# Kernel optimization log

Hardware: AMD Instinct MI355X
Metric: run time of the kernel (lower is better)

The kernel has to match this reference:

```python
import jax, jax.numpy as jnp
import numpy as np

VOCAB, SEQ, D_EMB, D_HID, BATCH = 50257, 256, 256, 512, 16

def setup_inputs() -> dict:
    key = jax.random.key(0)
    ks = jax.random.split(key, 8)
    s_e = 1.0 / np.sqrt(D_EMB)
    s_h = 1.0 / np.sqrt(D_HID)
    return {
        "idx": jax.random.randint(ks[0], (BATCH, SEQ), 0, VOCAB),
        "E":  jax.random.normal(ks[1], (VOCAB, D_EMB), jnp.float32) * 0.02,
        "Wi": jax.random.normal(ks[2], (D_EMB, 4 * D_HID), jnp.float32) * s_e,  # input kernel (no bias in flax LSTMCell)
        "Wh": jax.random.normal(ks[3], (D_HID, 4 * D_HID), jnp.float32) * s_h,  # recurrent kernel
        "bh": jnp.zeros((4 * D_HID,), jnp.float32),                              # recurrent bias
        "Wo": jax.random.normal(ks[4], (D_HID, VOCAB), jnp.float32) * s_h,
        "bo": jnp.zeros((VOCAB,), jnp.float32),
    }

def reference(idx, E, Wi, Wh, bh, Wo, bo):
    B, S = idx.shape
    H = Wh.shape[0]
    x = E[idx]                                   # [B, S, D] embedding gather
    # precompute input contribution for all timesteps: [S, B, 4H]
    xz = jnp.einsum('bsd,dg->sbg', x, Wi)

    def step(carry, xz_t):
        h, c = carry
        z = xz_t + h @ Wh + bh                   # [B, 4H]
        i, f, g, o = jnp.split(z, 4, axis=-1)    # flax gate order: i, f, g, o
        i = jax.nn.sigmoid(i)
        f = jax.nn.sigmoid(f)
        g = jnp.tanh(g)
        o = jax.nn.sigmoid(o)
        c = f * c + i * g
        h = o * jnp.tanh(c)
        return (h, c), h

    h0 = jnp.zeros((B, H), x.dtype)
    c0 = jnp.zeros((B, H), x.dtype)
    _, hs = jax.lax.scan(step, (h0, c0), xz)     # hs: [S, B, H]
    hs = jnp.transpose(hs, (1, 0, 2))            # [B, S, H]
    logits = hs @ Wo + bo                        # [B, S, V]
    return logits
```

## Files before the change

kernel.cpp:

```cpp
#include <hip/hip_runtime.h>
#include <cstdint>


typedef __attribute__((ext_vector_type(8))) short short8;
typedef __attribute__((ext_vector_type(4))) float f32x4;
typedef __attribute__((ext_vector_type(4))) unsigned int u32x4;
typedef __attribute__((ext_vector_type(4))) unsigned short ush4;

#define DEVFN static __device__ __forceinline__

DEVFN unsigned short f2bf(float f) {
    unsigned int u = __float_as_uint(f);
    return (unsigned short)((u + 0x7FFFu + ((u >> 16) & 1u)) >> 16);
}
DEVFN float bf2f(unsigned short h) { return __uint_as_float(((unsigned int)h) << 16); }
DEVFN float sigm(float x) { return 1.0f / (1.0f + __expf(-x)); }
DEVFN float tanh_fast(float x) {
    float e = __expf(-2.0f * fabsf(x));
    float t = (1.0f - e) / (1.0f + e);
    return copysignf(t, x);
}
DEVFN f32x4 fzero() { f32x4 v = {0.f, 0.f, 0.f, 0.f}; return v; }

DEVFN void aload16(u32x4& d, const void* p) {
    asm volatile("global_load_dwordx4 %0, %1, off sc0 sc1" : "=v"(d) : "v"(p));
}

__global__ __launch_bounds__(256) void k0_wot(const float* __restrict__ Wo,
                                              uint32_t* __restrict__ WoTP) {
    __shared__ float tile[32][33];
    const int bx = blockIdx.x;
    const int cb = bx >> 4;
    const int kb = bx & 15;
    const int c0 = cb * 32, k0 = kb * 32;
    const int j = threadIdx.x & 31;
    const int i0 = threadIdx.x >> 5;
    for (int ii = i0; ii < 32; ii += 8) {
        const int c = c0 + j;
        tile[ii][j] = (c < 50257) ? Wo[(size_t)(k0 + ii) * 50257 + c] : 0.0f;
    }
    __syncthreads();
    for (int ii = i0; ii < 32; ii += 8) {
        const float v = tile[j][ii];
        const unsigned short hi = f2bf(v);
        const unsigned short lo = f2bf(v - bf2f(hi));
        WoTP[(size_t)(c0 + ii) * 512 + k0 + j] = (((unsigned int)hi) << 16) | lo;
    }
}

__global__ __launch_bounds__(256) void k0b_whlo(const float* __restrict__ Wh,
                                                uint32_t* __restrict__ WLO) {
    const int tid = blockIdx.x * 256 + threadIdx.x;
    const int lane = tid & 63;
    const int q    = (tid >> 6) & 15;
    const int nt   = (tid >> 10) & 1;
    const int wg   = tid >> 11;
    const int cc   = lane & 15;
    const int gcol = (cc >> 2) * 512 + wg * 8 + nt * 4 + (cc & 3);
    const int kbase = q * 32 + (lane >> 4) * 8;
    u32x4 o;
#pragma unroll
    for (int p = 0; p < 4; ++p) {
        unsigned int pair = 0;
#pragma unroll
        for (int e = 0; e < 2; ++e) {
            const int k = kbase + p * 2 + e;
            const float w = Wh[(size_t)k * 2048 + gcol];
            const unsigned short hi = f2bf(w);
            const unsigned short lo = f2bf(w - bf2f(hi));
            pair |= ((unsigned int)lo) << (e * 16);
        }
        o[p] = pair;
    }
    *(u32x4*)(WLO + (size_t)tid * 4) = o;
}

__global__ __launch_bounds__(256) void k1_xz(const int* __restrict__ idx,
                                             const float* __restrict__ E,
                                             const float* __restrict__ Wi,
                                             unsigned short* __restrict__ xzH) {
    __shared__ float xs[16][256];
    const int s = blockIdx.x;
    const int t = threadIdx.x;
#pragma unroll
    for (int b = 0; b < 16; ++b) {
        const int row = idx[b * 256 + s];
        xs[b][t] = E[(size_t)row * 256 + t];
    }
    __syncthreads();
    for (int half = 0; half < 2; ++half) {
        const int g0 = half * 1024 + t * 4;
        f32x4 acc[16];
#pragma unroll
        for (int b = 0; b < 16; ++b) acc[b] = fzero();
        for (int d = 0; d < 256; ++d) {
            const f32x4 w = *(const f32x4*)&Wi[(size_t)d * 2048 + g0];
#pragma unroll
            for (int b = 0; b < 16; ++b) {
                const float xv = xs[b][d];
                acc[b] += xv * w;
            }
        }
#pragma unroll
        for (int b = 0; b < 16; ++b) {
            ush4 o;
#pragma unroll
            for (int jj = 0; jj < 4; ++jj) o[jj] = f2bf(acc[b][jj]);
            *(ush4*)&xzH[((size_t)s * 16 + b) * 2048 + g0] = o;
        }
    }
}

__global__ __launch_bounds__(256, 1) void k23(const float* __restrict__ Wh,
                                              const float* __restrict__ bh,
                                              const unsigned short* __restrict__ xzH,
                                              const short8* __restrict__ WLO8,
                                              uint32_t* __restrict__ hsP,
                                              const uint32_t* __restrict__ zeroh,
                                              uint32_t* __restrict__ flags,
                                              const uint32_t* __restrict__ WoTP,
                                              const float* __restrict__ bo,
                                              float* __restrict__ out) {
    __shared__ __align__(16) char smem[98304];

    if (blockIdx.x < 64) {
        const int wg = blockIdx.x;
        const int tid = threadIdx.x;

        unsigned short* whh = (unsigned short*)smem;

        {
            const int l = tid >> 3, seg = tid & 7;
            const int cc = l & 15, nt0 = l >> 4;
            const int gcol = (cc >> 2) * 512 + wg * 8 + nt0 * 4 + (cc & 3);
            for (int k8 = seg * 64; k8 < seg * 64 + 64; k8 += 8) {
                short8 v;
#pragma unroll
                for (int i = 0; i < 8; ++i)
                    v[i] = (short)f2bf(Wh[(size_t)(k8 + i) * 2048 + gcol]);
                const int slot = (k8 >> 3) ^ (l & 7);
                *(short8*)((char*)whh + l * 1024 + slot * 16) = v;
            }
        }
        __syncthreads();
        if (tid >= 64) return;

        const int lane = tid;
        const int c = lane & 15;
        const int qtr = lane >> 4;

        int gc[2];
        float bh_v[2];
#pragma unroll
        for (int nt = 0; nt < 2; ++nt) {
            gc[nt] = (c >> 2) * 512 + wg * 8 + nt * 4 + (c & 3);
            bh_v[nt] = bh[gc[nt]];
        }
        float cst[2][4];
#pragma unroll
        for (int nt = 0; nt < 2; ++nt)
#pragma unroll
            for (int r = 0; r < 4; ++r) cst[nt][r] = 0.0f;

        float xzv[2][4];
#pragma unroll
        for (int nt = 0; nt < 2; ++nt)
#pragma unroll
            for (int r = 0; r < 4; ++r)
                xzv[nt][r] = bf2f(xzH[(size_t)(qtr * 4 + r) * 2048 + gc[nt]]);

        const uint32_t* flg = flags + lane;

        short8 bz = {0, 0, 0, 0, 0, 0, 0, 0};
        f32x4 bd0 = fzero(), bd1 = fzero();

        for (int t = 0; t < 256; ++t) {
            if (t > 0) {
                while (true) {
                    const uint32_t v = __hip_atomic_load(flg, __ATOMIC_RELAXED,
                                                         __HIP_MEMORY_SCOPE_AGENT);
                    if (__all((int)(v >= (uint32_t)t))) break;
#pragma unroll
                    for (int i = 0; i < 4; ++i) {
                        bd0 = __builtin_amdgcn_mfma_f32_16x16x32_bf16(bz, bz, bd0, 0, 0, 0);
                        bd1 = __builtin_amdgcn_mfma_f32_16x16x32_bf16(bz, bz, bd1, 0, 0, 0);
                    }
                }
                __builtin_amdgcn_sched_barrier(0);
            }

            const uint32_t* hbase = (t == 0)
                ? (zeroh + (size_t)c * 512)
                : (hsP + ((size_t)(t - 1) * 16 + c) * 512);

            f32x4 acc[2][2];
#pragma unroll
            for (int nt = 0; nt < 2; ++nt) { acc[nt][0] = fzero(); acc[nt][1] = fzero(); }

#pragma unroll
            for (int q = 0; q < 16; ++q) {
                const int kb = q * 32 + qtr * 8;
                const unsigned long long* hb64 = (const unsigned long long*)(hbase + kb);
                unsigned long long d[4];
#pragma unroll
                for (int i = 0; i < 4; ++i)
                    d[i] = __hip_atomic_load(hb64 + i, __ATOMIC_RELAXED,
                                             __HIP_MEMORY_SCOPE_AGENT);
                short8 ahi, alo;
#pragma unroll
                for (int i = 0; i < 4; ++i) {
                    const uint32_t wlo32 = (uint32_t)d[i];
                    const uint32_t whi32 = (uint32_t)(d[i] >> 32);
                    ahi[2 * i]     = (short)(wlo32 >> 16); alo[2 * i]     = (short)(wlo32 & 0xffffu);
                    ahi[2 * i + 1] = (short)(whi32 >> 16); alo[2 * i + 1] = (short)(whi32 & 0xffffu);
                }
#pragma unroll
                for (int nt = 0; nt < 2; ++nt) {
                    const int l = nt * 16 + c;
                    const short8 bhi = *(const short8*)((const char*)whh + l * 1024 +
                                                        (((q * 4 + qtr) ^ (l & 7)) << 4));
                    const short8 blo = WLO8[(((size_t)wg * 2 + nt) * 16 + q) * 64 + lane];
                    f32x4 a = acc[nt][q & 1];
                    a = __builtin_amdgcn_mfma_f32_16x16x32_bf16(ahi, bhi, a, 0, 0, 0);
                    a = __builtin_amdgcn_mfma_f32_16x16x32_bf16(ahi, blo, a, 0, 0, 0);
                    a = __builtin_amdgcn_mfma_f32_16x16x32_bf16(alo, bhi, a, 0, 0, 0);
                    acc[nt][q & 1] = a;
                }
            }

#pragma unroll
            for (int nt = 0; nt < 2; ++nt) {
                f32x4 z4 = acc[nt][0] + acc[nt][1];
#pragma unroll
                for (int r = 0; r < 4; ++r) z4[r] += xzv[nt][r] + bh_v[nt];
#pragma unroll
                for (int r = 0; r < 4; ++r) {
                    const int sb = (lane & 0x33);
                    const float zi = __shfl(z4[r], sb);
                    const float zf = __shfl(z4[r], sb | 4);
                    const float zg = __shfl(z4[r], sb | 8);
                    const float zo = __shfl(z4[r], sb | 12);
                    const float iv = sigm(zi), fv = sigm(zf);
                    const float gv = tanh_fast(zg), ov = sigm(zo);
                    const float cv = fv * cst[nt][r] + iv * gv;
                    cst[nt][r] = cv;
                    const float hv = ov * tanh_fast(cv);
                    if ((c >> 2) == 0) {
                        const unsigned short hi = f2bf(hv);
                        const unsigned short lo = f2bf(hv - bf2f(hi));
                        const uint32_t packed = (((uint32_t)hi) << 16) | lo;
                        __hip_atomic_store(
                            &hsP[((size_t)t * 16 + qtr * 4 + r) * 512 + wg * 8 + nt * 4 + c],
                            packed, __ATOMIC_RELAXED, __HIP_MEMORY_SCOPE_AGENT);
                    }
                }
            }

            asm volatile("s_waitcnt vmcnt(0)" ::: "memory");
            if (lane == 0)
                __hip_atomic_store(&flags[wg], (uint32_t)(t + 1), __ATOMIC_RELAXED,
                                   __HIP_MEMORY_SCOPE_AGENT);

            if (t < 255) {
#pragma unroll
                for (int nt = 0; nt < 2; ++nt)
#pragma unroll
                    for (int r = 0; r < 4; ++r)
                        xzv[nt][r] = bf2f(xzH[((size_t)(t + 1) * 16 + qtr * 4 + r) * 2048 + gc[nt]]);
            }
        }
        asm volatile("" :: "v"(bd0), "v"(bd1));
    } else {
        unsigned short (*Ah)[64] = (unsigned short(*)[64])(smem);
        unsigned short (*Al)[64] = (unsigned short(*)[64])(smem + 16384);
        unsigned short (*Bh)[64] = (unsigned short(*)[64])(smem + 32768);
        unsigned short (*Bl)[64] = (unsigned short(*)[64])(smem + 49152);

        const int cid = blockIdx.x - 64;
        const int tid = threadIdx.x;
        const int lane = tid & 63;
        const int wv = tid >> 6;
        const int wr = wv >> 1, wc = wv & 1;
        const int srow = tid >> 1, shalf = tid & 1;

        short8 bz = {0, 0, 0, 0, 0, 0, 0, 0};
        f32x4 bd0 = fzero(), bd1 = fzero(), bd2 = fzero(), bd3 = fzero();

        for (int s0 = 0; s0 < 32; ++s0) {
            const unsigned need = (unsigned)(s0 * 8 + 8);
            while (true) {
                const unsigned f = __hip_atomic_load(&flags[lane], __ATOMIC_RELAXED,
                                                     __HIP_MEMORY_SCOPE_AGENT);
                if (__all((int)(f >= need))) break;
#pragma unroll
                for (int i = 0; i < 8; ++i) {
                    bd0 = __builtin_amdgcn_mfma_f32_16x16x32_bf16(bz, bz, bd0, 0, 0, 0);
                    bd1 = __builtin_amdgcn_mfma_f32_16x16x32_bf16(bz, bz, bd1, 0, 0, 0);
                    bd2 = __builtin_amdgcn_mfma_f32_16x16x32_bf16(bz, bz, bd2, 0, 0, 0);
                    bd3 = __builtin_amdgcn_mfma_f32_16x16x32_bf16(bz, bz, bd3, 0, 0, 0);
                }
            }

            for (int vi = 0; vi < 3; ++vi) {
                const int v = cid + vi * 192;
                if (v >= 393) break;

                f32x4 acc[4][4];
#pragma unroll
                for (int i = 0; i < 4; ++i)
#pragma unroll
                    for (int j = 0; j < 4; ++j) acc[i][j] = fzero();

                for (int kb = 0; kb < 8; ++kb) {
                    __syncthreads();
                    const uint32_t* sa = hsP + (size_t)(s0 * 128 + srow) * 512 + kb * 64 + shalf * 32;
                    const uint32_t* sbp = WoTP + (size_t)(v * 128 + srow) * 512 + kb * 64 + shalf * 32;
                    u32x4 av[8], bv[8];
#pragma unroll
                    for (int g = 0; g < 4; ++g) {
                        aload16(av[2 * g], sa + g * 8);
                        aload16(av[2 * g + 1], sa + g * 8 + 4);
                    }
#pragma unroll
                    for (int g = 0; g < 4; ++g) {
                        bv[2 * g]     = *(const u32x4*)(sbp + g * 8);
                        bv[2 * g + 1] = *(const u32x4*)(sbp + g * 8 + 4);
                    }
                    asm volatile("s_waitcnt vmcnt(0)" ::: "memory");
                    __builtin_amdgcn_sched_barrier(0);
#pragma unroll
                    for (int g = 0; g < 4; ++g) {
                        short8 hi, lo;
#pragma unroll
                        for (int i = 0; i < 4; ++i) {
                            hi[i]     = (short)(av[2 * g][i] >> 16);
                            lo[i]     = (short)(av[2 * g][i] & 0xffffu);
                            hi[4 + i] = (short)(av[2 * g + 1][i] >> 16);
                            lo[4 + i] = (short)(av[2 * g + 1][i] & 0xffffu);
                        }
                        const int sw = ((shalf * 4 + g) ^ (srow & 7)) << 4;
                        *(short8*)((char*)Ah + srow * 128 + sw) = hi;
                        *(short8*)((char*)Al + srow * 128 + sw) = lo;
                    }
#pragma unroll
                    for (int g = 0; g < 4; ++g) {
                        short8 hi, lo;
#pragma unroll
                        for (int i = 0; i < 4; ++i) {
                            hi[i]     = (short)(bv[2 * g][i] >> 16);
                            lo[i]     = (short)(bv[2 * g][i] & 0xffffu);
                            hi[4 + i] = (short)(bv[2 * g + 1][i] >> 16);
                            lo[4 + i] = (short)(bv[2 * g + 1][i] & 0xffffu);
                        }
                        const int sw = ((shalf * 4 + g) ^ (srow & 7)) << 4;
                        *(short8*)((char*)Bh + srow * 128 + sw) = hi;
                        *(short8*)((char*)Bl + srow * 128 + sw) = lo;
                    }
                    __syncthreads();

#pragma unroll
                    for (int q = 0; q < 2; ++q) {
                        short8 afh[4], afl[4], bfh[4], bfl[4];
#pragma unroll
                        for (int mi = 0; mi < 4; ++mi) {
                            const int r = wr * 64 + mi * 16 + (lane & 15);
                            const int sw = ((q * 4 + (lane >> 4)) ^ (r & 7)) << 4;
                            afh[mi] = *(const short8*)((const char*)Ah + r * 128 + sw);
                            afl[mi] = *(const short8*)((const char*)Al + r * 128 + sw);
                        }
#pragma unroll
                        for (int nj = 0; nj < 4; ++nj) {
                            const int r = wc * 64 + nj * 16 + (lane & 15);
                            const int sw = ((q * 4 + (lane >> 4)) ^ (r & 7)) << 4;
                            bfh[nj] = *(const short8*)((const char*)Bh + r * 128 + sw);
                            bfl[nj] = *(const short8*)((const char*)Bl + r * 128 + sw);
                        }
#pragma unroll
                        for (int mi = 0; mi < 4; ++mi)
#pragma unroll
                            for (int nj = 0; nj < 4; ++nj) {
                                f32x4 a = acc[mi][nj];
                                a = __builtin_amdgcn_mfma_f32_16x16x32_bf16(afh[mi], bfh[nj], a, 0, 0, 0);
                                a = __builtin_amdgcn_mfma_f32_16x16x32_bf16(afh[mi], bfl[nj], a, 0, 0, 0);
                                a = __builtin_amdgcn_mfma_f32_16x16x32_bf16(afl[mi], bfh[nj], a, 0, 0, 0);
                                acc[mi][nj] = a;
                            }
                    }
                }

#pragma unroll
                for (int nj = 0; nj < 4; ++nj) {
                    const int colg = v * 128 + wc * 64 + nj * 16 + (lane & 15);
                    if (colg < 50257) {
                        const float bov = bo[colg];
#pragma unroll
                        for (int mi = 0; mi < 4; ++mi)
#pragma unroll
                            for (int r = 0; r < 4; ++r) {
                                const int tr = wr * 64 + mi * 16 + (lane >> 4) * 4 + r;
                                const int ss = s0 * 8 + (tr >> 4);
                                const int bb = tr & 15;
                                out[((size_t)bb * 256 + ss) * 50257 + colg] = acc[mi][nj][r] + bov;
                            }
                    }
                }
            }
        }
        asm volatile("" :: "v"(bd0), "v"(bd1), "v"(bd2), "v"(bd3));
    }
}

#define XZH_OFF  0ull
#define HSP_OFF  16777216ull
#define ZERO_OFF 25165824ull
#define FLG_OFF  25198592ull
#define WLO_OFF  25198848ull
#define WOT_OFF  27296000ull

extern "C" void kernel_launch(void* const* d_in, const int* in_sizes, int n_in,
                              void* d_out, int out_size, void* d_ws, size_t ws_size,
                              hipStream_t stream) {
    (void)in_sizes; (void)n_in; (void)out_size; (void)ws_size;
    const int*   idx = (const int*)  d_in[0];
    const float* E   = (const float*)d_in[1];
    const float* Wi  = (const float*)d_in[2];
    const float* Wh  = (const float*)d_in[3];
    const float* bh  = (const float*)d_in[4];
    const float* Wo  = (const float*)d_in[5];
    const float* bo  = (const float*)d_in[6];
    float* out = (float*)d_out;
    char* ws = (char*)d_ws;

    unsigned short* xzH   = (unsigned short*)(ws + XZH_OFF);
    uint32_t*       hsP   = (uint32_t*)      (ws + HSP_OFF);
    uint32_t*       zeroh = (uint32_t*)      (ws + ZERO_OFF);
    uint32_t*       flags = (uint32_t*)      (ws + FLG_OFF);
    uint32_t*       WLO   = (uint32_t*)      (ws + WLO_OFF);
    uint32_t*       WoTP  = (uint32_t*)      (ws + WOT_OFF);

    hipMemsetAsync(ws + ZERO_OFF, 0, 33024, stream);

    hipLaunchKernelGGL(k0_wot,   dim3(25152), dim3(256), 0, stream, Wo, WoTP);
    hipLaunchKernelGGL(k0b_whlo, dim3(512),   dim3(256), 0, stream, Wh, WLO);
    hipLaunchKernelGGL(k1_xz,    dim3(256),   dim3(256), 0, stream, idx, E, Wi, xzH);
    hipLaunchKernelGGL(k23,      dim3(256),   dim3(256), 0, stream,
                       Wh, bh, xzH, (const short8*)WLO, hsP, zeroh, flags, WoTP, bo, out);
}
```

Before: 3.829 ms.

## Pack recurrence into 16 blocks with counter-based epoch barrier

The LSTM recurrence moves from 64 single-wave blocks to 16 blocks of 4 waves, each wave still owning one 8-column slice of Wh held in a larger LDS buffer. Per-slice flags are replaced by one global atomic counter that every block increments after each step. One wave per block polls it with MALL-bypassing loads and relays readiness through LDS, while block 0 publishes a coarse epoch for the output-projection blocks. This frees 48 CUs for the vocab GEMM, which now uses 240 consumer blocks with two tiles each, and it reduces polling traffic. The cost is a __syncthreads plus an atomic round trip on every timestep, contention on the single counter, and a relay hop that adds latency before the consumers see progress.

```diff
diff --git a/kernel.cpp b/kernel.cpp
--- a/kernel.cpp
+++ b/kernel.cpp
@@ -22,6 +22,15 @@
 }
 DEVFN f32x4 fzero() { f32x4 v = {0.f, 0.f, 0.f, 0.f}; return v; }
 
+DEVFN uint32_t ld_flag_mall(const uint32_t* p) {
+    uint32_t v;
+    asm volatile("global_load_dword %0, %1, off sc0 sc1\n\ts_waitcnt vmcnt(0)"
+                 : "=v"(v) : "v"(p) : "memory");
+    return v;
+}
+DEVFN void st_flag_mall(uint32_t* p, uint32_t v) {
+    asm volatile("global_store_dword %0, %1, off sc0 sc1" :: "v"(p), "v"(v) : "memory");
+}
 DEVFN void aload16(u32x4& d, const void* p) {
     asm volatile("global_load_dwordx4 %0, %1, off sc0 sc1" : "=v"(d) : "v"(p));
 }
@@ -54,9 +63,9 @@
     const int lane = tid & 63;
     const int q    = (tid >> 6) & 15;
     const int nt   = (tid >> 10) & 1;
-    const int wg   = tid >> 11;
+    const int vp   = tid >> 11;
     const int cc   = lane & 15;
-    const int gcol = (cc >> 2) * 512 + wg * 8 + nt * 4 + (cc & 3);
+    const int gcol = (cc >> 2) * 512 + vp * 8 + nt * 4 + (cc & 3);
     const int kbase = q * 32 + (lane >> 4) * 8;
     u32x4 o;
 #pragma unroll
@@ -117,35 +126,40 @@
                                               const short8* __restrict__ WLO8,
                                               uint32_t* __restrict__ hsP,
                                               const uint32_t* __restrict__ zeroh,
-                                              uint32_t* __restrict__ flags,
+                                              uint32_t* __restrict__ ep,
+                                              uint32_t* __restrict__ epC,
                                               const uint32_t* __restrict__ WoTP,
                                               const float* __restrict__ bo,
                                               float* __restrict__ out) {
-    __shared__ __align__(16) char smem[98304];
-
-    if (blockIdx.x < 64) {
-        const int wg = blockIdx.x;
-        const int tid = threadIdx.x;
-
-        unsigned short* whh = (unsigned short*)smem;
-
-        {
+    __shared__ __align__(16) char smem[131072];
+    __shared__ unsigned int sEp;
+
+    const int tid = threadIdx.x;
+
+    if (blockIdx.x < 16) {
+        const int blk = blockIdx.x;
+
+        for (int vs = 0; vs < 4; ++vs) {
+            const int vp_s = blk * 4 + vs;
             const int l = tid >> 3, seg = tid & 7;
             const int cc = l & 15, nt0 = l >> 4;
-            const int gcol = (cc >> 2) * 512 + wg * 8 + nt0 * 4 + (cc & 3);
+            const int gcol = (cc >> 2) * 512 + vp_s * 8 + nt0 * 4 + (cc & 3);
             for (int k8 = seg * 64; k8 < seg * 64 + 64; k8 += 8) {
                 short8 v;
 #pragma unroll
                 for (int i = 0; i < 8; ++i)
                     v[i] = (short)f2bf(Wh[(size_t)(k8 + i) * 2048 + gcol]);
                 const int slot = (k8 >> 3) ^ (l & 7);
-                *(short8*)((char*)whh + l * 1024 + slot * 16) = v;
-            }
-        }
+                *(short8*)(smem + vs * 32768 + l * 1024 + slot * 16) = v;
+            }
+        }
+        if (tid == 0) sEp = 0;
         __syncthreads();
-        if (tid >= 64) return;
-
-        const int lane = tid;
+
+        const int w = tid >> 6;
+        const int lane = tid & 63;
+        const int vp = blk * 4 + w;
+        unsigned short* whhW = (unsigned short*)(smem + w * 32768);
         const int c = lane & 15;
         const int qtr = lane >> 4;
 
@@ -153,7 +167,7 @@
         float bh_v[2];
 #pragma unroll
         for (int nt = 0; nt < 2; ++nt) {
-            gc[nt] = (c >> 2) * 512 + wg * 8 + nt * 4 + (c & 3);
+            gc[nt] = (c >> 2) * 512 + vp * 8 + nt * 4 + (c & 3);
             bh_v[nt] = bh[gc[nt]];
         }
         float cst[2][4];
@@ -169,22 +183,30 @@
             for (int r = 0; r < 4; ++r)
                 xzv[nt][r] = bf2f(xzH[(size_t)(qtr * 4 + r) * 2048 + gc[nt]]);
 
-        const uint32_t* flg = flags + lane;
-
         short8 bz = {0, 0, 0, 0, 0, 0, 0, 0};
         f32x4 bd0 = fzero(), bd1 = fzero();
 
         for (int t = 0; t < 256; ++t) {
             if (t > 0) {
-                while (true) {
-                    const uint32_t v = __hip_atomic_load(flg, __ATOMIC_RELAXED,
-                                                         __HIP_MEMORY_SCOPE_AGENT);
-                    if (__all((int)(v >= (uint32_t)t))) break;
-#pragma unroll
-                    for (int i = 0; i < 4; ++i) {
-                        bd0 = __builtin_amdgcn_mfma_f32_16x16x32_bf16(bz, bz, bd0, 0, 0, 0);
-                        bd1 = __builtin_amdgcn_mfma_f32_16x16x32_bf16(bz, bz, bd1, 0, 0, 0);
-                    }
+                const uint32_t tgt = 16u * (uint32_t)t;
+                if (w == 0) {
+                    while (true) {
+                        const uint32_t v = ld_flag_mall(ep);
+                        if (v >= tgt) break;
+#pragma unroll
+                        for (int i = 0; i < 2; ++i) {
+                            bd0 = __builtin_amdgcn_mfma_f32_16x16x32_bf16(bz, bz, bd0, 0, 0, 0);
+                            bd1 = __builtin_amdgcn_mfma_f32_16x16x32_bf16(bz, bz, bd1, 0, 0, 0);
+                        }
+                    }
+                    if (lane == 0) {
+                        __hip_atomic_store(&sEp, (unsigned)t, __ATOMIC_RELAXED,
+                                           __HIP_MEMORY_SCOPE_WORKGROUP);
+                        if (blk == 0) st_flag_mall(epC, (uint32_t)t);
+                    }
+                } else {
+                    while (__hip_atomic_load(&sEp, __ATOMIC_RELAXED,
+                                             __HIP_MEMORY_SCOPE_WORKGROUP) < (unsigned)t) {}
                 }
                 __builtin_amdgcn_sched_barrier(0);
             }
@@ -217,9 +239,9 @@
 #pragma unroll
                 for (int nt = 0; nt < 2; ++nt) {
                     const int l = nt * 16 + c;
-                    const short8 bhi = *(const short8*)((const char*)whh + l * 1024 +
+                    const short8 bhi = *(const short8*)((const char*)whhW + l * 1024 +
                                                         (((q * 4 + qtr) ^ (l & 7)) << 4));
-                    const short8 blo = WLO8[(((size_t)wg * 2 + nt) * 16 + q) * 64 + lane];
+                    const short8 blo = WLO8[(((size_t)vp * 2 + nt) * 16 + q) * 64 + lane];
                     f32x4 a = acc[nt][q & 1];
                     a = __builtin_amdgcn_mfma_f32_16x16x32_bf16(ahi, bhi, a, 0, 0, 0);
                     a = __builtin_amdgcn_mfma_f32_16x16x32_bf16(ahi, blo, a, 0, 0, 0);
@@ -250,16 +272,16 @@
                         const unsigned short lo = f2bf(hv - bf2f(hi));
                         const uint32_t packed = (((uint32_t)hi) << 16) | lo;
                         __hip_atomic_store(
-                            &hsP[((size_t)t * 16 + qtr * 4 + r) * 512 + wg * 8 + nt * 4 + c],
+                            &hsP[((size_t)t * 16 + qtr * 4 + r) * 512 + vp * 8 + nt * 4 + c],
                             packed, __ATOMIC_RELAXED, __HIP_MEMORY_SCOPE_AGENT);
                     }
                 }
             }
 
             asm volatile("s_waitcnt vmcnt(0)" ::: "memory");
-            if (lane == 0)
-                __hip_atomic_store(&flags[wg], (uint32_t)(t + 1), __ATOMIC_RELAXED,
-                                   __HIP_MEMORY_SCOPE_AGENT);
+            __syncthreads();
+            if (tid == 0)
+                __hip_atomic_fetch_add(ep, 1u, __ATOMIC_RELAXED, __HIP_MEMORY_SCOPE_AGENT);
 
             if (t < 255) {
 #pragma unroll
@@ -268,6 +290,11 @@
                     for (int r = 0; r < 4; ++r)
                         xzv[nt][r] = bf2f(xzH[((size_t)(t + 1) * 16 + qtr * 4 + r) * 2048 + gc[nt]]);
             }
+        }
+
+        if (blk == 0 && tid == 0) {
+            while (ld_flag_mall(ep) < 4096u) {}
+            st_flag_mall(epC, 256u);
         }
         asm volatile("" :: "v"(bd0), "v"(bd1));
     } else {
@@ -276,8 +303,7 @@
         unsigned short (*Bh)[64] = (unsigned short(*)[64])(smem + 32768);
         unsigned short (*Bl)[64] = (unsigned short(*)[64])(smem + 49152);
 
-        const int cid = blockIdx.x - 64;
-        const int tid = threadIdx.x;
+        const int cid = blockIdx.x - 16;
         const int lane = tid & 63;
         const int wv = tid >> 6;
         const int wr = wv >> 1, wc = wv & 1;
@@ -289,9 +315,8 @@
         for (int s0 = 0; s0 < 32; ++s0) {
             const unsigned need = (unsigned)(s0 * 8 + 8);
             while (true) {
-                const unsigned f = __hip_atomic_load(&flags[lane], __ATOMIC_RELAXED,
-                                                     __HIP_MEMORY_SCOPE_AGENT);
-                if (__all((int)(f >= need))) break;
+                const uint32_t f = ld_flag_mall(epC);
+                if (f >= need) break;
 #pragma unroll
                 for (int i = 0; i < 8; ++i) {
                     bd0 = __builtin_amdgcn_mfma_f32_16x16x32_bf16(bz, bz, bd0, 0, 0, 0);
@@ -301,8 +326,8 @@
                 }
             }
 
-            for (int vi = 0; vi < 3; ++vi) {
-                const int v = cid + vi * 192;
+            for (int vi = 0; vi < 2; ++vi) {
+                const int v = cid + vi * 240;
                 if (v >= 393) break;
 
                 f32x4 acc[4][4];
@@ -410,12 +435,12 @@
     }
 }
 
-#define XZH_OFF  0ull
-#define HSP_OFF  16777216ull
-#define ZERO_OFF 25165824ull
-#define FLG_OFF  25198592ull
-#define WLO_OFF  25198848ull
-#define WOT_OFF  27296000ull
+#define XZH_OFF   0ull
+#define HSP_OFF   16777216ull
+#define ZEROH_OFF 25165824ull
+#define FLG_OFF   25198592ull
+#define WLO_OFF   25198848ull
+#define WOT_OFF   27296000ull
 
 extern "C" void kernel_launch(void* const* d_in, const int* in_sizes, int n_in,
                               void* d_out, int out_size, void* d_ws, size_t ws_size,
@@ -433,16 +458,17 @@
 
     unsigned short* xzH   = (unsigned short*)(ws + XZH_OFF);
     uint32_t*       hsP   = (uint32_t*)      (ws + HSP_OFF);
-    uint32_t*       zeroh = (uint32_t*)      (ws + ZERO_OFF);
-    uint32_t*       flags = (uint32_t*)      (ws + FLG_OFF);
+    uint32_t*       zeroh = (uint32_t*)      (ws + ZEROH_OFF);
+    uint32_t*       ep    = (uint32_t*)      (ws + FLG_OFF);
+    uint32_t*       epC   = (uint32_t*)      (ws + FLG_OFF + 128);
     uint32_t*       WLO   = (uint32_t*)      (ws + WLO_OFF);
     uint32_t*       WoTP  = (uint32_t*)      (ws + WOT_OFF);
 
-    hipMemsetAsync(ws + ZERO_OFF, 0, 33024, stream);
+    hipMemsetAsync(ws + ZEROH_OFF, 0, 33024, stream);
 
     hipLaunchKernelGGL(k0_wot,   dim3(25152), dim3(256), 0, stream, Wo, WoTP);
     hipLaunchKernelGGL(k0b_whlo, dim3(512),   dim3(256), 0, stream, Wh, WLO);
     hipLaunchKernelGGL(k1_xz,    dim3(256),   dim3(256), 0, stream, idx, E, Wi, xzH);
     hipLaunchKernelGGL(k23,      dim3(256),   dim3(256), 0, stream,
-                       Wh, bh, xzH, (const short8*)WLO, hsP, zeroh, flags, WoTP, bo, out);
-}
+                       Wh, bh, xzH, (const short8*)WLO, hsP, zeroh, ep, epC, WoTP, bo, out);
+}
```

Measured after the change: 3.347 ms. 12.6% less time.
